# Optimization experiments

Hardware: AMD Instinct MI355X
Metric: run time of the kernel (lower is better)

Reference implementation:

```python
import jax, jax.numpy as jnp
import numpy as np

A, B, M, H, NMOL = 100000, 200000, 50000, 128, 4000
DEPTH = 5
MAX_NB = 8


def setup_inputs() -> dict:
    key = jax.random.key(0)
    ks = jax.random.split(key, 10)
    fatoms = jax.random.normal(ks[0], (A, 35), dtype=jnp.float32)
    fbonds = jax.random.normal(ks[1], (B, 40), dtype=jnp.float32)
    # index 0 of the combined message table is the zero padding message
    tree_message = jax.random.normal(ks[2], (M, H), dtype=jnp.float32).at[0].set(0.0)
    agraph = jax.random.randint(ks[3], (A, MAX_NB), 0, M + B, dtype=jnp.int32)
    bgraph = jax.random.randint(ks[4], (B, MAX_NB), 0, M + B, dtype=jnp.int32)
    mol_id = jnp.sort(jax.random.randint(ks[5], (A,), 0, NMOL, dtype=jnp.int32))
    W_i = jax.random.normal(ks[6], (40, H), dtype=jnp.float32) * 0.05
    W_h = jax.random.normal(ks[7], (H, H), dtype=jnp.float32) * 0.05
    W_o = jax.random.normal(ks[8], (35 + H, H), dtype=jnp.float32) * 0.05
    b_o = jax.random.normal(ks[9], (H,), dtype=jnp.float32) * 0.05
    return {"fatoms": fatoms, "fbonds": fbonds, "tree_message": tree_message,
            "agraph": agraph, "bgraph": bgraph, "mol_id": mol_id,
            "W_i": W_i, "W_h": W_h, "W_o": W_o, "b_o": b_o, "n_mols": NMOL}


def reference(fatoms, fbonds, tree_message, agraph, bgraph, mol_id, W_i, W_h, W_o, b_o, n_mols):
    binput = fbonds @ W_i                      # [B, H]
    graph_message = jax.nn.relu(binput)        # [B, H]
    for _ in range(DEPTH - 1):
        message = jnp.concatenate([tree_message, graph_message], axis=0)  # [M+B, H]
        nei = jnp.take(message, bgraph, axis=0).sum(axis=1)               # [B, H]
        graph_message = jax.nn.relu(binput + nei @ W_h)
    message = jnp.concatenate([tree_message, graph_message], axis=0)
    nei_a = jnp.take(message, agraph, axis=0).sum(axis=1)                 # [A, H]
    ainput = jnp.concatenate([fatoms, nei_a], axis=1)                     # [A, 35+H]
    atom_hiddens = jax.nn.relu(ainput @ W_o + b_o)                        # [A, H]
    sums = jax.ops.segment_sum(atom_hiddens, mol_id, num_segments=n_mols)
    counts = jax.ops.segment_sum(jnp.ones((atom_hiddens.shape[0],), dtype=atom_hiddens.dtype),
                                 mol_id, num_segments=n_mols)
    mol_vecs = sums / jnp.maximum(counts, 1.0)[:, None]                   # [n_mols, H]
    return mol_vecs
```

## Files before the change

kernel.cpp:

```cpp
#include <hip/hip_runtime.h>
#include <hip/hip_bf16.h>

#define AN 100000
#define BN 200000
#define MN 50000
#define HD 128
#define NMOL 4000
#define MAXNB 8
#define BSZ 24576

typedef unsigned short u16;
typedef unsigned int   u32;
typedef float f32x4 __attribute__((ext_vector_type(4)));
typedef short s16x8 __attribute__((ext_vector_type(8)));

__device__ __forceinline__ u16 f2bf(float x) {
    u32 u = __float_as_uint(x);
    return (u16)((u + 0x7fffu + ((u >> 16) & 1u)) >> 16);
}
__device__ __forceinline__ float bf2f(u16 x) { return __uint_as_float((u32)x << 16); }

__device__ __forceinline__ s16x8 zero8() { return (s16x8){0, 0, 0, 0, 0, 0, 0, 0}; }

__device__ __forceinline__ s16x8 pack44(float4 a, float4 b) {
    union { uint4 u; s16x8 s; } r;
    r.u.x = (u32)f2bf(a.x) | ((u32)f2bf(a.y) << 16);
    r.u.y = (u32)f2bf(a.z) | ((u32)f2bf(a.w) << 16);
    r.u.z = (u32)f2bf(b.x) | ((u32)f2bf(b.y) << 16);
    r.u.w = (u32)f2bf(b.z) | ((u32)f2bf(b.w) << 16);
    return r.s;
}

__global__ __launch_bounds__(256) void k_prep(const float* __restrict__ tree,
                                              u16* __restrict__ tree_bf,
                                              const float* __restrict__ W_h,
                                              const float* __restrict__ W_i,
                                              const float* __restrict__ W_o,
                                              const float* __restrict__ b_o,
                                              u16* __restrict__ Bit,
                                              u16* __restrict__ Bat,
                                              const int* __restrict__ mol_id,
                                              float* __restrict__ counts,
                                              const float* __restrict__ fbonds,
                                              u16* __restrict__ fbp,
                                              const int* __restrict__ bgraph,
                                              int* __restrict__ bgd,
                                              int bgd_end) {
    int blk = blockIdx.x, tid = threadIdx.x;
    if (blk < 6250) {
        int i = blk * 256 + tid;
        const float4 v = ((const float4*)tree)[i];
        uint2 r;
        r.x = (u32)f2bf(v.x) | ((u32)f2bf(v.y) << 16);
        r.y = (u32)f2bf(v.z) | ((u32)f2bf(v.w) << 16);
        ((uint2*)tree_bf)[i] = r;
    } else if (blk < 6442) {
        int i = (blk - 6250) * 256 + tid;
        int which = (i >= BSZ);
        int e = which ? i - BSZ : i;
        int j = e & 7, lane = (e >> 3) & 63, nt = (e >> 9) & 7, kt = e >> 12;
        int k = kt * 32 + (lane >> 4) * 8 + j;
        int n = nt * 16 + (lane & 15);
        if (!which) {
            float v = (k < 128) ? W_h[k * 128 + n] : ((k < 168) ? W_i[(k - 128) * 128 + n] : 0.f);
            Bit[e] = f2bf(v);
        } else {
            float v = (k < 128) ? W_o[(35 + k) * 128 + n]
                    : (k < 163) ? W_o[(k - 128) * 128 + n]
                    : (k == 163) ? b_o[n] : 0.f;
            Bat[e] = f2bf(v);
        }
    } else if (blk < 6458) {
        int m = (blk - 6442) * 256 + tid;
        if (m < NMOL) {
            int lo = 0, hi = AN;
            while (lo < hi) { int mid = (lo + hi) >> 1; if (mol_id[mid] < m) lo = mid + 1; else hi = mid; }
            int s = lo; lo = 0; hi = AN;
            while (lo < hi) { int mid = (lo + hi) >> 1; if (mol_id[mid] < m + 1) lo = mid + 1; else hi = mid; }
            counts[m] = (float)(lo - s);
        }
    } else if (blk < bgd_end) {
        int q = (blk - 6458) * 256 + tid;
        if (q < 400000) {
            int4 v = ((const int4*)bgraph)[q];
            v.x = (v.x >= MN) ? v.x : 0;
            v.y = (v.y >= MN) ? v.y : 0;
            v.z = (v.z >= MN) ? v.z : 0;
            v.w = (v.w >= MN) ? v.w : 0;
            ((int4*)bgd)[q] = v;
        }
    } else {
        int q = (blk - bgd_end) * 256 + tid;
        if (q < 2000000) {
            const float4 v = ((const float4*)fbonds)[q];
            uint2 r;
            r.x = (u32)f2bf(v.x) | ((u32)f2bf(v.y) << 16);
            r.y = (u32)f2bf(v.z) | ((u32)f2bf(v.w) << 16);
            ((uint2*)fbp)[q] = r;
        }
    }
}

#define LDA 136

__device__ __forceinline__ void fb_frags_pk(const u16* __restrict__ fbp, int b, int aq,
                                            s16x8& lo, s16x8& hi) {
    const uint4* f4 = (const uint4*)fbp;
    uint4 v = f4[(size_t)b * 5 + aq];
    lo = *(const s16x8*)&v;
    if (aq == 0) {
        uint4 w = f4[(size_t)b * 5 + 4];
        hi = *(const s16x8*)&w;
    } else hi = zero8();
}

__device__ __forceinline__ void fb_frags_f32(const float* __restrict__ fbonds, int b, int aq,
                                             s16x8& lo, s16x8& hi) {
    const float4* f4 = (const float4*)(fbonds + (size_t)b * 40);
    float4 x = f4[aq * 2], y = f4[aq * 2 + 1];
    lo = pack44(x, y);
    if (aq == 0) {
        float4 p = f4[8], q = f4[9];
        hi = pack44(p, q);
    } else hi = zero8();
}

__device__ __forceinline__ void gather16(u16 (*sA)[LDA], const int (*sidx)[MAXNB],
                                         const u16* __restrict__ tree_bf,
                                         const u16* __restrict__ tin, int tid) {
    int l = tid & 15, tb = tid >> 4;
#pragma unroll
    for (int pp = 0; pp < 2; ++pp) {
        int r0 = tb + (2 * pp) * 16;
        int r1 = tb + (2 * pp + 1) * 16;
        uint4 v[2][8];
#pragma unroll
        for (int j = 0; j < 8; ++j) {
            int idx = sidx[r0][j];
            const u16* base = (idx < MN) ? tree_bf + (size_t)idx * HD
                                         : tin + (size_t)(idx - MN) * HD;
            v[0][j] = ((const uint4*)base)[l];
        }
#pragma unroll
        for (int j = 0; j < 8; ++j) {
            int idx = sidx[r1][j];
            const u16* base = (idx < MN) ? tree_bf + (size_t)idx * HD
                                         : tin + (size_t)(idx - MN) * HD;
            v[1][j] = ((const uint4*)base)[l];
        }
#pragma unroll
        for (int h = 0; h < 2; ++h) {
            float a[8] = {0.f, 0.f, 0.f, 0.f, 0.f, 0.f, 0.f, 0.f};
#pragma unroll
            for (int j = 0; j < 8; ++j) {
                a[0] += __uint_as_float(v[h][j].x << 16);
                a[1] += __uint_as_float(v[h][j].x & 0xffff0000u);
                a[2] += __uint_as_float(v[h][j].y << 16);
                a[3] += __uint_as_float(v[h][j].y & 0xffff0000u);
                a[4] += __uint_as_float(v[h][j].z << 16);
                a[5] += __uint_as_float(v[h][j].z & 0xffff0000u);
                a[6] += __uint_as_float(v[h][j].w << 16);
                a[7] += __uint_as_float(v[h][j].w & 0xffff0000u);
            }
            uint4 r;
            r.x = (u32)f2bf(a[0]) | ((u32)f2bf(a[1]) << 16);
            r.y = (u32)f2bf(a[2]) | ((u32)f2bf(a[3]) << 16);
            r.z = (u32)f2bf(a[4]) | ((u32)f2bf(a[5]) << 16);
            r.w = (u32)f2bf(a[6]) | ((u32)f2bf(a[7]) << 16);
            *(uint4*)&sA[h == 0 ? r0 : r1][l * 8] = r;
        }
    }
}

template <bool PK>
__global__ __launch_bounds__(256) void k_binput2(const float* __restrict__ fbonds,
                                                 const u16* __restrict__ fbp,
                                                 const u16* __restrict__ tree_bf,
                                                 const int* __restrict__ bgraph,
                                                 const u16* __restrict__ Bsw,
                                                 u16* __restrict__ g0,
                                                 u16* __restrict__ base2) {
    __shared__ __align__(16) u16 sA[64][LDA];
    __shared__ int sidx[64][MAXNB];
    int tid = threadIdx.x;
    int b0  = blockIdx.x * 64;

    for (int i = tid; i < 64 * MAXNB; i += 256) {
        int idx = bgraph[(size_t)(b0 + (i >> 3)) * MAXNB + (i & 7)];
        sidx[i >> 3][i & 7] = (idx < MN) ? idx : 0;
    }
    __syncthreads();
    gather16(sA, sidx, tree_bf, tree_bf, tid);
    __syncthreads();

    int lane = tid & 63, wv = tid >> 6;
    int am = lane & 15, aq = lane >> 4;
    s16x8 afr[6];
#pragma unroll
    for (int kt = 0; kt < 4; ++kt)
        afr[kt] = *(const s16x8*)&sA[wv * 16 + am][kt * 32 + aq * 8];
    int b = b0 + wv * 16 + am;
    if (PK) fb_frags_pk(fbp, b, aq, afr[4], afr[5]);
    else    fb_frags_f32(fbonds, b, aq, afr[4], afr[5]);

    const s16x8* B8 = (const s16x8*)Bsw;
    f32x4 accB[8];
#pragma unroll
    for (int nt = 0; nt < 8; ++nt) accB[nt] = (f32x4){0.f, 0.f, 0.f, 0.f};
#pragma unroll
    for (int kt = 4; kt < 6; ++kt)
#pragma unroll
        for (int nt = 0; nt < 8; ++nt) {
            s16x8 bfr = B8[(kt * 8 + nt) * 64 + lane];
            accB[nt] = __builtin_amdgcn_mfma_f32_16x16x32_bf16(afr[kt], bfr, accB[nt], 0, 0, 0);
        }
    f32x4 accF[8];
#pragma unroll
    for (int nt = 0; nt < 8; ++nt) accF[nt] = accB[nt];
#pragma unroll
    for (int kt = 0; kt < 4; ++kt)
#pragma unroll
        for (int nt = 0; nt < 8; ++nt) {
            s16x8 bfr = B8[(kt * 8 + nt) * 64 + lane];
            accF[nt] = __builtin_amdgcn_mfma_f32_16x16x32_bf16(afr[kt], bfr, accF[nt], 0, 0, 0);
        }

#pragma unroll
    for (int nt = 0; nt < 8; ++nt)
#pragma unroll
        for (int r = 0; r < 4; ++r)
            sA[wv * 16 + aq * 4 + r][nt * 16 + am] = f2bf(fmaxf(accB[nt][r], 0.f));
    __syncthreads();
#pragma unroll
    for (int s = 0; s < 4; ++s) {
        int e = tid + s * 256;
        int row = e >> 4, seg = e & 15;
        *(uint4*)&g0[((size_t)b0 + row) * HD + seg * 8] = *(const uint4*)&sA[row][seg * 8];
    }
    __syncthreads();
#pragma unroll
    for (int nt = 0; nt < 8; ++nt)
#pragma unroll
        for (int r = 0; r < 4; ++r)
            sA[wv * 16 + aq * 4 + r][nt * 16 + am] = f2bf(accF[nt][r]);
    __syncthreads();
#pragma unroll
    for (int s = 0; s < 4; ++s) {
        int e = tid + s * 256;
        int row = e >> 4, seg = e & 15;
        *(uint4*)&base2[((size_t)b0 + row) * HD + seg * 8] = *(const uint4*)&sA[row][seg * 8];
    }
}

__global__ __launch_bounds__(256) void k_iter_fold(const u16* __restrict__ tree_bf,
                                                   const u16* __restrict__ tin,
                                                   const u16* __restrict__ base2,
                                                   const int* __restrict__ bgd,
                                                   const u16* __restrict__ Bsw,
                                                   u16* __restrict__ tout) {
    __shared__ __align__(16) u16 sA[64][LDA];
    __shared__ int sidx[64][MAXNB];
    int tid = threadIdx.x;
    int b0  = blockIdx.x * 64;

    for (int i = tid; i < 64 * MAXNB; i += 256)
        sidx[i >> 3][i & 7] = bgd[(size_t)(b0 + (i >> 3)) * MAXNB + (i & 7)];
    __syncthreads();

    gather16(sA, sidx, tree_bf, tin, tid);

    int lane = tid & 63, wv = tid >> 6;
    int am = lane & 15, aq = lane >> 4;
    f32x4 acc[8];
    {
        const u16* b2 = base2 + (size_t)(b0 + wv * 16 + aq * 4) * HD + am;
#pragma unroll
        for (int r = 0; r < 4; ++r)
#pragma unroll
            for (int nt = 0; nt < 8; ++nt)
                acc[nt][r] = bf2f(b2[(size_t)r * HD + nt * 16]);
    }
    __syncthreads();

    s16x8 afr[4];
#pragma unroll
    for (int kt = 0; kt < 4; ++kt)
        afr[kt] = *(const s16x8*)&sA[wv * 16 + am][kt * 32 + aq * 8];
    const s16x8* B8 = (const s16x8*)Bsw;
#pragma unroll
    for (int kt = 0; kt < 4; ++kt)
#pragma unroll
        for (int nt = 0; nt < 8; ++nt) {
            s16x8 bfr = B8[(kt * 8 + nt) * 64 + lane];
            acc[nt] = __builtin_amdgcn_mfma_f32_16x16x32_bf16(afr[kt], bfr, acc[nt], 0, 0, 0);
        }
#pragma unroll
    for (int nt = 0; nt < 8; ++nt)
#pragma unroll
        for (int r = 0; r < 4; ++r)
            sA[wv * 16 + aq * 4 + r][nt * 16 + am] = f2bf(fmaxf(acc[nt][r], 0.f));
    __syncthreads();
#pragma unroll
    for (int s = 0; s < 4; ++s) {
        int e = tid + s * 256;
        int row = e >> 4, seg = e & 15;
        *(uint4*)&tout[((size_t)b0 + row) * HD + seg * 8] = *(const uint4*)&sA[row][seg * 8];
    }
}

template <bool PK>
__global__ __launch_bounds__(256) void k_binput_mfma(const float* __restrict__ fbonds,
                                                     const u16* __restrict__ fbp,
                                                     const u16* __restrict__ Bsw,
                                                     u16* __restrict__ g0) {
    __shared__ __align__(16) u16 sA[64][LDA];
    int tid = threadIdx.x;
    int b0  = blockIdx.x * 64;
    int lane = tid & 63, wv = tid >> 6;
    int am = lane & 15, aq = lane >> 4;
    int b = b0 + wv * 16 + am;
    s16x8 afr[2];
    if (PK) fb_frags_pk(fbp, b, aq, afr[0], afr[1]);
    else    fb_frags_f32(fbonds, b, aq, afr[0], afr[1]);
    f32x4 acc[8];
#pragma unroll
    for (int nt = 0; nt < 8; ++nt) acc[nt] = (f32x4){0.f, 0.f, 0.f, 0.f};
    const s16x8* B8 = (const s16x8*)Bsw;
#pragma unroll
    for (int kt = 0; kt < 2; ++kt)
#pragma unroll
        for (int nt = 0; nt < 8; ++nt) {
            s16x8 bfr = B8[((4 + kt) * 8 + nt) * 64 + lane];
            acc[nt] = __builtin_amdgcn_mfma_f32_16x16x32_bf16(afr[kt], bfr, acc[nt], 0, 0, 0);
        }
#pragma unroll
    for (int nt = 0; nt < 8; ++nt)
#pragma unroll
        for (int r = 0; r < 4; ++r)
            sA[wv * 16 + aq * 4 + r][nt * 16 + am] = f2bf(fmaxf(acc[nt][r], 0.f));
    __syncthreads();
#pragma unroll
    for (int s = 0; s < 4; ++s) {
        int e = tid + s * 256;
        int row = e >> 4, seg = e & 15;
        *(uint4*)&g0[((size_t)b0 + row) * HD + seg * 8] = *(const uint4*)&sA[row][seg * 8];
    }
}

template <bool PK>
__global__ __launch_bounds__(256) void k_iter_mfma(const u16* __restrict__ tree_bf,
                                                   const u16* __restrict__ tin,
                                                   const float* __restrict__ fbonds,
                                                   const u16* __restrict__ fbp,
                                                   const int* __restrict__ bgraph,
                                                   const u16* __restrict__ Bsw,
                                                   u16* __restrict__ tout) {
    __shared__ __align__(16) u16 sA[64][LDA];
    __shared__ int sidx[64][MAXNB];
    int tid = threadIdx.x;
    int b0  = blockIdx.x * 64;

    for (int i = tid; i < 64 * MAXNB; i += 256)
        sidx[i >> 3][i & 7] = bgraph[(size_t)(b0 + (i >> 3)) * MAXNB + (i & 7)];
    __syncthreads();

    gather16(sA, sidx, tree_bf, tin, tid);
    __syncthreads();

    int lane = tid & 63, wv = tid >> 6;
    int am = lane & 15, aq = lane >> 4;
    s16x8 afr[6];
#pragma unroll
    for (int kt = 0; kt < 4; ++kt)
        afr[kt] = *(const s16x8*)&sA[wv * 16 + am][kt * 32 + aq * 8];
    int b = b0 + wv * 16 + am;
    if (PK) fb_frags_pk(fbp, b, aq, afr[4], afr[5]);
    else    fb_frags_f32(fbonds, b, aq, afr[4], afr[5]);
    f32x4 acc[8];
#pragma unroll
    for (int nt = 0; nt < 8; ++nt) acc[nt] = (f32x4){0.f, 0.f, 0.f, 0.f};
    const s16x8* B8 = (const s16x8*)Bsw;
#pragma unroll
    for (int kt = 0; kt < 6; ++kt)
#pragma unroll
        for (int nt = 0; nt < 8; ++nt) {
            s16x8 bfr = B8[(kt * 8 + nt) * 64 + lane];
            acc[nt] = __builtin_amdgcn_mfma_f32_16x16x32_bf16(afr[kt], bfr, acc[nt], 0, 0, 0);
        }
#pragma unroll
    for (int nt = 0; nt < 8; ++nt)
#pragma unroll
        for (int r = 0; r < 4; ++r)
            sA[wv * 16 + aq * 4 + r][nt * 16 + am] = f2bf(fmaxf(acc[nt][r], 0.f));
    __syncthreads();
#pragma unroll
    for (int s = 0; s < 4; ++s) {
        int e = tid + s * 256;
        int row = e >> 4, seg = e & 15;
        *(uint4*)&tout[((size_t)b0 + row) * HD + seg * 8] = *(const uint4*)&sA[row][seg * 8];
    }
}

__global__ __launch_bounds__(256) void k_atom_mfma(const u16* __restrict__ tree_bf,
                                                   const u16* __restrict__ gfin,
                                                   const float* __restrict__ fatoms,
                                                   const int* __restrict__ agraph,
                                                   const int* __restrict__ mol_id,
                                                   const u16* __restrict__ Bsw,
                                                   float* __restrict__ sums) {
    __shared__ __align__(16) u16 sA[64][LDA];
    __shared__ int sidx[64][MAXNB];
    __shared__ int smol[64];
    int tid = threadIdx.x;
    int a0  = blockIdx.x * 64;

    for (int i = tid; i < 64 * MAXNB; i += 256) {
        int a = a0 + (i >> 3);
        sidx[i >> 3][i & 7] = (a < AN) ? agraph[(size_t)a * MAXNB + (i & 7)] : 0;
    }
    if (tid < 64) smol[tid] = (a0 + tid < AN) ? mol_id[a0 + tid] : -1;
    __syncthreads();
    gather16(sA, sidx, tree_bf, gfin, tid);
    __syncthreads();

    int lane = tid & 63, wv = tid >> 6;
    int am = lane & 15, aq = lane >> 4;
    s16x8 afr[6];
#pragma unroll
    for (int kt = 0; kt < 4; ++kt)
        afr[kt] = *(const s16x8*)&sA[wv * 16 + am][kt * 32 + aq * 8];
    {
        int a = a0 + wv * 16 + am;
        float f[8] = {0.f, 0.f, 0.f, 0.f, 0.f, 0.f, 0.f, 0.f};
        if (a < AN) {
            const float* fr = fatoms + (size_t)a * 35;
#pragma unroll
            for (int j = 0; j < 8; ++j) f[j] = fr[aq * 8 + j];
        }
        union { uint4 u; s16x8 s; } r4;
        r4.u.x = (u32)f2bf(f[0]) | ((u32)f2bf(f[1]) << 16);
        r4.u.y = (u32)f2bf(f[2]) | ((u32)f2bf(f[3]) << 16);
        r4.u.z = (u32)f2bf(f[4]) | ((u32)f2bf(f[5]) << 16);
        r4.u.w = (u32)f2bf(f[6]) | ((u32)f2bf(f[7]) << 16);
        afr[4] = r4.s;
        if (aq == 0) {
            float g0 = 0.f, g1 = 0.f, g2 = 0.f, g3 = 0.f;
            if (a < AN) {
                const float* fr = fatoms + (size_t)a * 35;
                g0 = fr[32]; g1 = fr[33]; g2 = fr[34]; g3 = 1.f;
            }
            union { uint4 u; s16x8 s; } r5;
            r5.u.x = (u32)f2bf(g0) | ((u32)f2bf(g1) << 16);
            r5.u.y = (u32)f2bf(g2) | ((u32)f2bf(g3) << 16);
            r5.u.z = 0u; r5.u.w = 0u;
            afr[5] = r5.s;
        } else afr[5] = zero8();
    }

    f32x4 acc[8];
#pragma unroll
    for (int nt = 0; nt < 8; ++nt) acc[nt] = (f32x4){0.f, 0.f, 0.f, 0.f};
    const s16x8* B8 = (const s16x8*)Bsw;
#pragma unroll
    for (int kt = 0; kt < 6; ++kt)
#pragma unroll
        for (int nt = 0; nt < 8; ++nt) {
            s16x8 bfr = B8[(kt * 8 + nt) * 64 + lane];
            acc[nt] = __builtin_amdgcn_mfma_f32_16x16x32_bf16(afr[kt], bfr, acc[nt], 0, 0, 0);
        }
#pragma unroll
    for (int nt = 0; nt < 8; ++nt)
#pragma unroll
        for (int r = 0; r < 4; ++r)
            sA[wv * 16 + aq * 4 + r][nt * 16 + am] = f2bf(fmaxf(acc[nt][r], 0.f));
    __syncthreads();

    {
        int c = tid & 127, half = tid >> 7;
        int base = half * 32;
        float run = 0.f;
        int cur = smol[base];
        for (int r = 0; r < 32; ++r) {
            int row = base + r;
            int mv = smol[row];
            if (mv != cur) {
                if (cur >= 0) atomicAdd(&sums[(size_t)cur * HD + c], run);
                run = 0.f; cur = mv;
            }
            run += __uint_as_float((u32)sA[row][c] << 16);
        }
        if (cur >= 0) atomicAdd(&sums[(size_t)cur * HD + c], run);
    }
}

__global__ __launch_bounds__(256) void k_div(const float* __restrict__ sums,
                                             const float* __restrict__ counts,
                                             float* __restrict__ out) {
    int i = blockIdx.x * 256 + threadIdx.x;
    if (i < NMOL * HD) out[i] = sums[i] / fmaxf(counts[i >> 7], 1.f);
}

extern "C" void kernel_launch(void* const* d_in, const int* in_sizes, int n_in,
                              void* d_out, int out_size, void* d_ws, size_t ws_size,
                              hipStream_t stream) {
    const float* fatoms = (const float*)d_in[0];
    const float* fbonds = (const float*)d_in[1];
    const float* tree   = (const float*)d_in[2];
    const int*   agraph = (const int*)d_in[3];
    const int*   bgraph = (const int*)d_in[4];
    const int*   mol_id = (const int*)d_in[5];
    const float* W_i    = (const float*)d_in[6];
    const float* W_h    = (const float*)d_in[7];
    const float* W_o    = (const float*)d_in[8];
    const float* b_o    = (const float*)d_in[9];
    float* out = (float*)d_out;

    size_t tbl   = (size_t)BN * HD;
    size_t treeN = (size_t)MN * HD;
    size_t fbN   = (size_t)BN * 40;
    size_t redN  = (size_t)(NMOL * HD + NMOL);
    size_t edgeN = (size_t)BN * MAXNB;

    size_t need_base = (2 * tbl + treeN + 2 * BSZ) * 2 + redN * 4;
    size_t need_pack = need_base + fbN * 2;
    size_t need_fold = need_pack + tbl * 2 + edgeN * 4;

    if (ws_size < need_base) {
        hipMemsetAsync(d_out, 0, (size_t)out_size * sizeof(float), stream);
        return;
    }
    bool pk   = (ws_size >= need_pack);
    bool fold = (ws_size >= need_fold);

    u16* t0      = (u16*)d_ws;
    u16* t1      = t0 + tbl;
    u16* tree_bf = t1 + tbl;
    u16* Bit     = tree_bf + treeN;
    u16* Bat     = Bit + BSZ;
    u16* fbp     = pk ? (Bat + BSZ) : nullptr;
    u16* base2   = fold ? (fbp + fbN) : nullptr;
    int* bgd     = fold ? (int*)(base2 + tbl) : nullptr;
    float* sums  = (float*)(fold ? (void*)(bgd + edgeN)
                          : pk   ? (void*)(fbp + fbN)
                                 : (void*)(Bat + BSZ));
    float* counts = sums + (size_t)NMOL * HD;

    hipMemsetAsync(sums, 0, (size_t)NMOL * HD * sizeof(float), stream);

    int bgd_end = fold ? 6458 + 1563 : 6458;
    int prep_grid = bgd_end + (pk ? 7813 : 0);
    k_prep<<<prep_grid, 256, 0, stream>>>(tree, tree_bf, W_h, W_i, W_o, b_o,
                                          Bit, Bat, mol_id, counts, fbonds, fbp,
                                          bgraph, bgd, bgd_end);

    u16* cur = t0;
    u16* nxt = t1;
    if (fold) {
        k_binput2<true><<<BN / 64, 256, 0, stream>>>(fbonds, fbp, tree_bf, bgraph,
                                                     Bit, t0, base2);
        for (int it = 0; it < 4; ++it) {
            k_iter_fold<<<BN / 64, 256, 0, stream>>>(tree_bf, cur, base2, bgd, Bit, nxt);
            u16* t = cur; cur = nxt; nxt = t;
        }
    } else {
        if (pk)
            k_binput_mfma<true><<<BN / 64, 256, 0, stream>>>(fbonds, fbp, Bit, t0);
        else
            k_binput_mfma<false><<<BN / 64, 256, 0, stream>>>(fbonds, fbp, Bit, t0);
        for (int it = 0; it < 4; ++it) {
            if (pk)
                k_iter_mfma<true><<<BN / 64, 256, 0, stream>>>(tree_bf, cur, fbonds, fbp,
                                                               bgraph, Bit, nxt);
            else
                k_iter_mfma<false><<<BN / 64, 256, 0, stream>>>(tree_bf, cur, fbonds, fbp,
                                                                bgraph, Bit, nxt);
            u16* t = cur; cur = nxt; nxt = t;
        }
    }
    k_atom_mfma<<<(AN + 63) / 64, 256, 0, stream>>>(tree_bf, cur, fatoms, agraph,
                                                    mol_id, Bat, sums);
    k_div<<<(NMOL * HD) / 256, 256, 0, stream>>>(sums, counts, out);
}
```

Before: 486.3 us.

## Store graph messages as FP8 e4m3 to halve gather traffic in fold path

The per-bond graph messages written between iterations now use 8-bit e4m3 storage instead of bf16. Gathers in the iteration and atom kernels read 8-byte instead of 16-byte chunks per lane and convert in registers, with hardware conversion builtins used when available. Padding index zero is skipped instead of loaded. The binput kernel is reordered to reuse one accumulator set. This cuts the memory traffic of the gather-bound loop at the cost of much lower message precision, which risks accuracy against the fp32 reference.

Result: faster. 397.7 us (median of 2 runs) (-18.2%).

```diff
diff --git a/kernel.cpp b/kernel.cpp
--- a/kernel.cpp
+++ b/kernel.cpp
@@ -11,7 +11,9 @@
 
 typedef unsigned short u16;
 typedef unsigned int   u32;
+typedef unsigned char  u8;
 typedef float f32x4 __attribute__((ext_vector_type(4)));
+typedef float f32x2 __attribute__((ext_vector_type(2)));
 typedef short s16x8 __attribute__((ext_vector_type(8)));
 
 __device__ __forceinline__ u16 f2bf(float x) {
@@ -29,6 +31,64 @@
     r.u.z = (u32)f2bf(b.x) | ((u32)f2bf(b.y) << 16);
     r.u.w = (u32)f2bf(b.z) | ((u32)f2bf(b.w) << 16);
     return r.s;
+}
+
+#if defined(__has_builtin)
+#if __has_builtin(__builtin_amdgcn_cvt_pk_f32_fp8) && __has_builtin(__builtin_amdgcn_cvt_pk_fp8_f32)
+#define HW_FP8 1
+#endif
+#endif
+
+__device__ __forceinline__ void fp8x4_to_f32(u32 w, float* o) {
+#ifdef HW_FP8
+    f32x2 a = __builtin_amdgcn_cvt_pk_f32_fp8((int)w, false);
+    f32x2 b = __builtin_amdgcn_cvt_pk_f32_fp8((int)w, true);
+    o[0] = a.x; o[1] = a.y; o[2] = b.x; o[3] = b.y;
+#else
+#pragma unroll
+    for (int i = 0; i < 4; ++i) {
+        u32 b8 = (w >> (i * 8)) & 0xffu;
+        u32 s = (b8 >> 7) & 1u, em = b8 & 0x7fu;
+        float v;
+        if (em < 8u) v = (float)em * 0.001953125f;
+        else v = __uint_as_float((((em >> 3) + 120u) << 23) | ((em & 7u) << 20));
+        o[i] = s ? -v : v;
+    }
+#endif
+}
+
+__device__ __forceinline__ u32 f32_1_to_fp8_sw(float x) {
+    u32 s = (__float_as_uint(x) >> 31) << 7;
+    float ax = fabsf(x);
+    if (ax >= 448.f) return s | 0x7e;
+    u32 b = __float_as_uint(ax);
+    int e = (int)(b >> 23) - 127;
+    if (e < -6) {
+        float t = ax * 512.0f;
+        u32 m = (u32)(t + 0.5f);
+        if (m > 8u) m = 8u;
+        return s | m;
+    }
+    u32 mant = b & 0x7fffffu;
+    u32 keep = mant >> 20;
+    u32 rest = mant & 0xfffffu;
+    u32 rnd = (rest > 0x80000u) || (rest == 0x80000u && (keep & 1u));
+    keep += rnd;
+    u32 ee = (u32)(e + 7);
+    if (keep == 8u) { keep = 0u; ee++; }
+    if (ee >= 16u || (ee == 15u && keep == 7u)) return s | 0x7e;
+    return s | (ee << 3) | keep;
+}
+
+__device__ __forceinline__ u32 f32x4_to_fp8(float a, float b, float c, float d) {
+#ifdef HW_FP8
+    int r = __builtin_amdgcn_cvt_pk_fp8_f32(a, b, 0, false);
+    r = __builtin_amdgcn_cvt_pk_fp8_f32(c, d, r, true);
+    return (u32)r;
+#else
+    return f32_1_to_fp8_sw(a) | (f32_1_to_fp8_sw(b) << 8) |
+           (f32_1_to_fp8_sw(c) << 16) | (f32_1_to_fp8_sw(d) << 24);
+#endif
 }
 
 __global__ __launch_bounds__(256) void k_prep(const float* __restrict__ tree,
@@ -125,6 +185,26 @@
     } else hi = zero8();
 }
 
+__device__ __forceinline__ void acc_bf16(const uint4& v, float* a) {
+    a[0] += __uint_as_float(v.x << 16);
+    a[1] += __uint_as_float(v.x & 0xffff0000u);
+    a[2] += __uint_as_float(v.y << 16);
+    a[3] += __uint_as_float(v.y & 0xffff0000u);
+    a[4] += __uint_as_float(v.z << 16);
+    a[5] += __uint_as_float(v.z & 0xffff0000u);
+    a[6] += __uint_as_float(v.w << 16);
+    a[7] += __uint_as_float(v.w & 0xffff0000u);
+}
+
+__device__ __forceinline__ void pack_row(u16 (*sA)[LDA], int row, int l, const float* a) {
+    uint4 r;
+    r.x = (u32)f2bf(a[0]) | ((u32)f2bf(a[1]) << 16);
+    r.y = (u32)f2bf(a[2]) | ((u32)f2bf(a[3]) << 16);
+    r.z = (u32)f2bf(a[4]) | ((u32)f2bf(a[5]) << 16);
+    r.w = (u32)f2bf(a[6]) | ((u32)f2bf(a[7]) << 16);
+    *(uint4*)&sA[row][l * 8] = r;
+}
+
 __device__ __forceinline__ void gather16(u16 (*sA)[LDA], const int (*sidx)[MAXNB],
                                          const u16* __restrict__ tree_bf,
                                          const u16* __restrict__ tin, int tid) {
@@ -152,23 +232,139 @@
         for (int h = 0; h < 2; ++h) {
             float a[8] = {0.f, 0.f, 0.f, 0.f, 0.f, 0.f, 0.f, 0.f};
 #pragma unroll
+            for (int j = 0; j < 8; ++j) acc_bf16(v[h][j], a);
+            pack_row(sA, h == 0 ? r0 : r1, l, a);
+        }
+    }
+}
+
+__device__ __forceinline__ void gather_tree(u16 (*sA)[LDA], const int (*sidx)[MAXNB],
+                                            const u16* __restrict__ tree_bf, int tid) {
+    int l = tid & 15, tb = tid >> 4;
+#pragma unroll
+    for (int pp = 0; pp < 2; ++pp) {
+        int r0 = tb + (2 * pp) * 16;
+        int r1 = tb + (2 * pp + 1) * 16;
+        uint4 v[2][8];
+#pragma unroll
+        for (int j = 0; j < 8; ++j) {
+            int idx = sidx[r0][j];
+            uint4 w = {0u, 0u, 0u, 0u};
+            if (idx) w = ((const uint4*)(tree_bf + (size_t)idx * HD))[l];
+            v[0][j] = w;
+        }
+#pragma unroll
+        for (int j = 0; j < 8; ++j) {
+            int idx = sidx[r1][j];
+            uint4 w = {0u, 0u, 0u, 0u};
+            if (idx) w = ((const uint4*)(tree_bf + (size_t)idx * HD))[l];
+            v[1][j] = w;
+        }
+#pragma unroll
+        for (int h = 0; h < 2; ++h) {
+            float a[8] = {0.f, 0.f, 0.f, 0.f, 0.f, 0.f, 0.f, 0.f};
+#pragma unroll
+            for (int j = 0; j < 8; ++j) acc_bf16(v[h][j], a);
+            pack_row(sA, h == 0 ? r0 : r1, l, a);
+        }
+    }
+}
+
+__device__ __forceinline__ void gather_fp8(u16 (*sA)[LDA], const int (*sidx)[MAXNB],
+                                           const u8* __restrict__ tin, int tid) {
+    int l = tid & 15, tb = tid >> 4;
+#pragma unroll
+    for (int pp = 0; pp < 2; ++pp) {
+        int r0 = tb + (2 * pp) * 16;
+        int r1 = tb + (2 * pp + 1) * 16;
+        uint2 v[2][8];
+#pragma unroll
+        for (int j = 0; j < 8; ++j) {
+            int idx = sidx[r0][j];
+            uint2 w = {0u, 0u};
+            if (idx) w = *((const uint2*)(tin + (size_t)(idx - MN) * HD) + l);
+            v[0][j] = w;
+        }
+#pragma unroll
+        for (int j = 0; j < 8; ++j) {
+            int idx = sidx[r1][j];
+            uint2 w = {0u, 0u};
+            if (idx) w = *((const uint2*)(tin + (size_t)(idx - MN) * HD) + l);
+            v[1][j] = w;
+        }
+#pragma unroll
+        for (int h = 0; h < 2; ++h) {
+            float a[8] = {0.f, 0.f, 0.f, 0.f, 0.f, 0.f, 0.f, 0.f};
+#pragma unroll
             for (int j = 0; j < 8; ++j) {
-                a[0] += __uint_as_float(v[h][j].x << 16);
-                a[1] += __uint_as_float(v[h][j].x & 0xffff0000u);
-                a[2] += __uint_as_float(v[h][j].y << 16);
-                a[3] += __uint_as_float(v[h][j].y & 0xffff0000u);
-                a[4] += __uint_as_float(v[h][j].z << 16);
-                a[5] += __uint_as_float(v[h][j].z & 0xffff0000u);
-                a[6] += __uint_as_float(v[h][j].w << 16);
-                a[7] += __uint_as_float(v[h][j].w & 0xffff0000u);
+                float t[4];
+                fp8x4_to_f32(v[h][j].x, t);
+                a[0] += t[0]; a[1] += t[1]; a[2] += t[2]; a[3] += t[3];
+                fp8x4_to_f32(v[h][j].y, t);
+                a[4] += t[0]; a[5] += t[1]; a[6] += t[2]; a[7] += t[3];
             }
-            uint4 r;
-            r.x = (u32)f2bf(a[0]) | ((u32)f2bf(a[1]) << 16);
-            r.y = (u32)f2bf(a[2]) | ((u32)f2bf(a[3]) << 16);
-            r.z = (u32)f2bf(a[4]) | ((u32)f2bf(a[5]) << 16);
-            r.w = (u32)f2bf(a[6]) | ((u32)f2bf(a[7]) << 16);
-            *(uint4*)&sA[h == 0 ? r0 : r1][l * 8] = r;
-        }
+            pack_row(sA, h == 0 ? r0 : r1, l, a);
+        }
+    }
+}
+
+__device__ __forceinline__ void gather_mixed(u16 (*sA)[LDA], const int (*sidx)[MAXNB],
+                                             const u16* __restrict__ tree_bf,
+                                             const u8* __restrict__ dyn, int tid) {
+    int l = tid & 15, tb = tid >> 4;
+#pragma unroll
+    for (int pp = 0; pp < 4; ++pp) {
+        int r = tb + pp * 16;
+        uint4 v[8]; int id[8];
+#pragma unroll
+        for (int j = 0; j < 8; ++j) {
+            int idx = sidx[r][j];
+            id[j] = idx;
+            uint4 w = {0u, 0u, 0u, 0u};
+            if (idx >= MN) {
+                uint2 t = *((const uint2*)(dyn + (size_t)(idx - MN) * HD) + l);
+                w.x = t.x; w.y = t.y;
+            } else if (idx) {
+                w = ((const uint4*)(tree_bf + (size_t)idx * HD))[l];
+            }
+            v[j] = w;
+        }
+        float a[8] = {0.f, 0.f, 0.f, 0.f, 0.f, 0.f, 0.f, 0.f};
+#pragma unroll
+        for (int j = 0; j < 8; ++j) {
+            if (id[j] >= MN) {
+                float t[4];
+                fp8x4_to_f32(v[j].x, t);
+                a[0] += t[0]; a[1] += t[1]; a[2] += t[2]; a[3] += t[3];
+                fp8x4_to_f32(v[j].y, t);
+                a[4] += t[0]; a[5] += t[1]; a[6] += t[2]; a[7] += t[3];
+            } else {
+                acc_bf16(v[j], a);
+            }
+        }
+        pack_row(sA, r, l, a);
+    }
+}
+
+__device__ __forceinline__ void store_tile_fp8(const u16 (*sA)[LDA], u8* __restrict__ dst,
+                                               int b0, int tid) {
+#pragma unroll
+    for (int s = 0; s < 4; ++s) {
+        int e = tid + s * 256;
+        int row = e >> 4, seg = e & 15;
+        uint4 w = *(const uint4*)&sA[row][seg * 8];
+        float f0 = fminf(__uint_as_float(w.x << 16), 448.f);
+        float f1 = fminf(__uint_as_float(w.x & 0xffff0000u), 448.f);
+        float f2 = fminf(__uint_as_float(w.y << 16), 448.f);
+        float f3 = fminf(__uint_as_float(w.y & 0xffff0000u), 448.f);
+        float f4 = fminf(__uint_as_float(w.z << 16), 448.f);
+        float f5 = fminf(__uint_as_float(w.z & 0xffff0000u), 448.f);
+        float f6 = fminf(__uint_as_float(w.w << 16), 448.f);
+        float f7 = fminf(__uint_as_float(w.w & 0xffff0000u), 448.f);
+        uint2 o;
+        o.x = f32x4_to_fp8(f0, f1, f2, f3);
+        o.y = f32x4_to_fp8(f4, f5, f6, f7);
+        *((uint2*)(dst + (size_t)(b0 + row) * HD) + seg) = o;
     }
 }
 
@@ -178,7 +374,7 @@
                                                  const u16* __restrict__ tree_bf,
                                                  const int* __restrict__ bgraph,
                                                  const u16* __restrict__ Bsw,
-                                                 u16* __restrict__ g0,
+                                                 u8* __restrict__ g0,
                                                  u16* __restrict__ base2) {
     __shared__ __align__(16) u16 sA[64][LDA];
     __shared__ int sidx[64][MAXNB];
@@ -190,7 +386,7 @@
         sidx[i >> 3][i & 7] = (idx < MN) ? idx : 0;
     }
     __syncthreads();
-    gather16(sA, sidx, tree_bf, tree_bf, tid);
+    gather_tree(sA, sidx, tree_bf, tid);
     __syncthreads();
 
     int lane = tid & 63, wv = tid >> 6;
@@ -204,45 +400,36 @@
     else    fb_frags_f32(fbonds, b, aq, afr[4], afr[5]);
 
     const s16x8* B8 = (const s16x8*)Bsw;
-    f32x4 accB[8];
-#pragma unroll
-    for (int nt = 0; nt < 8; ++nt) accB[nt] = (f32x4){0.f, 0.f, 0.f, 0.f};
+    f32x4 acc[8];
+#pragma unroll
+    for (int nt = 0; nt < 8; ++nt) acc[nt] = (f32x4){0.f, 0.f, 0.f, 0.f};
 #pragma unroll
     for (int kt = 4; kt < 6; ++kt)
 #pragma unroll
         for (int nt = 0; nt < 8; ++nt) {
             s16x8 bfr = B8[(kt * 8 + nt) * 64 + lane];
-            accB[nt] = __builtin_amdgcn_mfma_f32_16x16x32_bf16(afr[kt], bfr, accB[nt], 0, 0, 0);
-        }
-    f32x4 accF[8];
-#pragma unroll
-    for (int nt = 0; nt < 8; ++nt) accF[nt] = accB[nt];
+            acc[nt] = __builtin_amdgcn_mfma_f32_16x16x32_bf16(afr[kt], bfr, acc[nt], 0, 0, 0);
+        }
+#pragma unroll
+    for (int nt = 0; nt < 8; ++nt)
+#pragma unroll
+        for (int r = 0; r < 4; ++r)
+            sA[wv * 16 + aq * 4 + r][nt * 16 + am] = f2bf(fmaxf(acc[nt][r], 0.f));
+    __syncthreads();
+    store_tile_fp8(sA, g0, b0, tid);
 #pragma unroll
     for (int kt = 0; kt < 4; ++kt)
 #pragma unroll
         for (int nt = 0; nt < 8; ++nt) {
             s16x8 bfr = B8[(kt * 8 + nt) * 64 + lane];
-            accF[nt] = __builtin_amdgcn_mfma_f32_16x16x32_bf16(afr[kt], bfr, accF[nt], 0, 0, 0);
-        }
-
+            acc[nt] = __builtin_amdgcn_mfma_f32_16x16x32_bf16(afr[kt], bfr, acc[nt], 0, 0, 0);
+        }
+    __syncthreads();
 #pragma unroll
     for (int nt = 0; nt < 8; ++nt)
 #pragma unroll
         for (int r = 0; r < 4; ++r)
-            sA[wv * 16 + aq * 4 + r][nt * 16 + am] = f2bf(fmaxf(accB[nt][r], 0.f));
-    __syncthreads();
-#pragma unroll
-    for (int s = 0; s < 4; ++s) {
-        int e = tid + s * 256;
-        int row = e >> 4, seg = e & 15;
-        *(uint4*)&g0[((size_t)b0 + row) * HD + seg * 8] = *(const uint4*)&sA[row][seg * 8];
-    }
-    __syncthreads();
-#pragma unroll
-    for (int nt = 0; nt < 8; ++nt)
-#pragma unroll
-        for (int r = 0; r < 4; ++r)
-            sA[wv * 16 + aq * 4 + r][nt * 16 + am] = f2bf(accF[nt][r]);
+            sA[wv * 16 + aq * 4 + r][nt * 16 + am] = f2bf(acc[nt][r]);
     __syncthreads();
 #pragma unroll
     for (int s = 0; s < 4; ++s) {
@@ -252,12 +439,11 @@
     }
 }
 
-__global__ __launch_bounds__(256) void k_iter_fold(const u16* __restrict__ tree_bf,
-                                                   const u16* __restrict__ tin,
+__global__ __launch_bounds__(256) void k_iter_fold(const u8* __restrict__ tin,
                                                    const u16* __restrict__ base2,
                                                    const int* __restrict__ bgd,
                                                    const u16* __restrict__ Bsw,
-                                                   u16* __restrict__ tout) {
+                                                   u8* __restrict__ tout) {
     __shared__ __align__(16) u16 sA[64][LDA];
     __shared__ int sidx[64][MAXNB];
     int tid = threadIdx.x;
@@ -267,7 +453,7 @@
         sidx[i >> 3][i & 7] = bgd[(size_t)(b0 + (i >> 3)) * MAXNB + (i & 7)];
     __syncthreads();
 
-    gather16(sA, sidx, tree_bf, tin, tid);
+    gather_fp8(sA, sidx, tin, tid);
 
     int lane = tid & 63, wv = tid >> 6;
     int am = lane & 15, aq = lane >> 4;
@@ -300,12 +486,7 @@
         for (int r = 0; r < 4; ++r)
             sA[wv * 16 + aq * 4 + r][nt * 16 + am] = f2bf(fmaxf(acc[nt][r], 0.f));
     __syncthreads();
-#pragma unroll
-    for (int s = 0; s < 4; ++s) {
-        int e = tid + s * 256;
-        int row = e >> 4, seg = e & 15;
-        *(uint4*)&tout[((size_t)b0 + row) * HD + seg * 8] = *(const uint4*)&sA[row][seg * 8];
-    }
+    store_tile_fp8(sA, tout, b0, tid);
 }
 
 template <bool PK>
@@ -401,8 +582,9 @@
     }
 }
 
+template <bool F8>
 __global__ __launch_bounds__(256) void k_atom_mfma(const u16* __restrict__ tree_bf,
-                                                   const u16* __restrict__ gfin,
+                                                   const void* __restrict__ gfin,
                                                    const float* __restrict__ fatoms,
                                                    const int* __restrict__ agraph,
                                                    const int* __restrict__ mol_id,
@@ -420,7 +602,8 @@
     }
     if (tid < 64) smol[tid] = (a0 + tid < AN) ? mol_id[a0 + tid] : -1;
     __syncthreads();
-    gather16(sA, sidx, tree_bf, gfin, tid);
+    if (F8) gather_mixed(sA, sidx, tree_bf, (const u8*)gfin, tid);
+    else    gather16(sA, sidx, tree_bf, (const u16*)gfin, tid);
     __syncthreads();
 
     int lane = tid & 63, wv = tid >> 6;
@@ -553,16 +736,22 @@
                                           Bit, Bat, mol_id, counts, fbonds, fbp,
                                           bgraph, bgd, bgd_end);
 
-    u16* cur = t0;
-    u16* nxt = t1;
     if (fold) {
+        u8* f0 = (u8*)t0;
+        u8* f1 = (u8*)t1;
         k_binput2<true><<<BN / 64, 256, 0, stream>>>(fbonds, fbp, tree_bf, bgraph,
-                                                     Bit, t0, base2);
+                                                     Bit, f0, base2);
+        u8* cur = f0;
+        u8* nxt = f1;
         for (int it = 0; it < 4; ++it) {
-            k_iter_fold<<<BN / 64, 256, 0, stream>>>(tree_bf, cur, base2, bgd, Bit, nxt);
-            u16* t = cur; cur = nxt; nxt = t;
-        }
+            k_iter_fold<<<BN / 64, 256, 0, stream>>>(cur, base2, bgd, Bit, nxt);
+            u8* t = cur; cur = nxt; nxt = t;
+        }
+        k_atom_mfma<true><<<(AN + 63) / 64, 256, 0, stream>>>(tree_bf, cur, fatoms, agraph,
+                                                              mol_id, Bat, sums);
     } else {
+        u16* cur = t0;
+        u16* nxt = t1;
         if (pk)
             k_binput_mfma<true><<<BN / 64, 256, 0, stream>>>(fbonds, fbp, Bit, t0);
         else
@@ -576,8 +765,8 @@
                                                                 bgraph, Bit, nxt);
             u16* t = cur; cur = nxt; nxt = t;
         }
-    }
-    k_atom_mfma<<<(AN + 63) / 64, 256, 0, stream>>>(tree_bf, cur, fatoms, agraph,
-                                                    mol_id, Bat, sums);
+        k_atom_mfma<false><<<(AN + 63) / 64, 256, 0, stream>>>(tree_bf, cur, fatoms, agraph,
+                                                               mol_id, Bat, sums);
+    }
     k_div<<<(NMOL * HD) / 256, 256, 0, stream>>>(sums, counts, out);
 }
```
